# Kernel tuning notes

Hardware: AMD Instinct MI355X
Metric: run time of the kernel (lower is better)

The kernel has to match this reference:

```python
import jax, jax.numpy as jnp
import numpy as np

D_QK = 32  # out_channels // 8


def conv1x1(x, w, b):
    # x: [B,C,H,W], w: [O,C], b: [O] -> [B,O,H,W]
    return jnp.einsum('bchw,oc->bohw', x, w) + b[None, :, None, None]


def setup_inputs() -> dict:
    key = jax.random.key(0)
    ks = jax.random.split(key, 10)
    B, C, H, W = 4, 256, 64, 64
    in_ch, out_ch, attn_ch = 512, 256, 256
    s_in = 1.0 / np.sqrt(in_ch)
    s_at = 1.0 / np.sqrt(attn_ch)
    return {
        'ef': jax.random.normal(ks[0], (B, C, H, W), jnp.float32),
        'sf': jax.random.normal(ks[1], (B, C, H, W), jnp.float32),
        'Attn': jax.random.normal(ks[2], (B, attn_ch, H, W), jnp.float32),
        'Qw': jax.random.uniform(ks[3], (D_QK, in_ch), jnp.float32, -s_in, s_in),
        'Qb': jax.random.uniform(ks[4], (D_QK,), jnp.float32, -s_in, s_in),
        'Kw': jax.random.uniform(ks[5], (D_QK, attn_ch), jnp.float32, -s_at, s_at),
        'Kb': jax.random.uniform(ks[6], (D_QK,), jnp.float32, -s_at, s_at),
        'Vw': jax.random.uniform(ks[7], (out_ch, in_ch), jnp.float32, -s_in, s_in),
        'Vb': jax.random.uniform(ks[8], (out_ch,), jnp.float32, -s_in, s_in),
        'gamma': jnp.ones((1,), jnp.float32) * 0.25,
    }


def reference(ef, sf, Attn, Qw, Qb, Kw, Kb, Vw, Vb, gamma):
    B, C, H, W = ef.shape
    N = H * W
    x = jnp.concatenate((ef, sf), axis=1)  # [B, 2C, H, W]
    q = conv1x1(x, Qw, Qb).reshape(B, D_QK, N)         # [B, d, N]
    k = conv1x1(Attn, Kw, Kb).reshape(B, D_QK, N)      # [B, d, N]
    # scores[b, m, n] = sum_d q[b, d, m] * k[b, d, n]  (no 1/sqrt(d) scale)
    scores = jnp.einsum('bdm,bdn->bmn', q, k)
    attn = jax.nn.softmax(scores, axis=-1)             # [B, N, N]
    v = conv1x1(x, Vw, Vb).reshape(B, C, N)            # [B, C, N]
    # out[b, c, m] = sum_n v[b, c, n] * attn[b, m, n]
    out = jnp.einsum('bcn,bmn->bcm', v, attn).reshape(B, C, H, W)
    return gamma[0] * out + ef
```

## Files before the change

kernel.cpp:

```cpp
#include <hip/hip_runtime.h>
#include <hip/hip_bf16.h>

typedef short bf16x8 __attribute__((ext_vector_type(8)));
typedef float f32x4 __attribute__((ext_vector_type(4)));

#define MFMA16(a, b, c) __builtin_amdgcn_mfma_f32_16x16x32_bf16(a, b, c, 0, 0, 0)

#define NB 4
#define NC 256
#define NSP 4096
#define LOG2E 1.4426950408889634f

__device__ __forceinline__ unsigned short f2bf(float f) {
    return (unsigned short)((__float_as_uint(f) + 0x8000u) >> 16);
}
__device__ __forceinline__ unsigned pk2bf(float hi, float lo) {
    return __builtin_amdgcn_perm(__float_as_uint(hi) + 0x8000u,
                                 __float_as_uint(lo) + 0x8000u, 0x07060302u);
}

__global__ __launch_bounds__(256) void prep_w(
    const float* __restrict__ Qw, const float* __restrict__ Kw,
    const float* __restrict__ Vw,
    unsigned short* __restrict__ Qwbf, unsigned short* __restrict__ Kwbf,
    unsigned short* __restrict__ Vwbf)
{
    int i = blockIdx.x * 256 + threadIdx.x;
    {
        const float4* vs = (const float4*)(Vw + (size_t)i * 8);
        float4 a = vs[0], c = vs[1];
        int4 st;
        st.x = (int)pk2bf(a.y, a.x); st.y = (int)pk2bf(a.w, a.z);
        st.z = (int)pk2bf(c.y, c.x); st.w = (int)pk2bf(c.w, c.z);
        *(int4*)(Vwbf + (size_t)i * 8) = st;
    }
    if (i < 2048) {
        const float4* qs = (const float4*)(Qw + (size_t)i * 8);
        float4 a = qs[0], c = qs[1];
        int4 st;
        st.x = (int)pk2bf(a.y, a.x); st.y = (int)pk2bf(a.w, a.z);
        st.z = (int)pk2bf(c.y, c.x); st.w = (int)pk2bf(c.w, c.z);
        *(int4*)(Qwbf + (size_t)i * 8) = st;
    }
    if (i < 1024) {
        const float4* ks = (const float4*)(Kw + (size_t)i * 8);
        float4 a = ks[0], c = ks[1];
        int4 st;
        st.x = (int)pk2bf(a.y, a.x); st.y = (int)pk2bf(a.w, a.z);
        st.z = (int)pk2bf(c.y, c.x); st.w = (int)pk2bf(c.w, c.z);
        *(int4*)(Kwbf + (size_t)i * 8) = st;
    }
}

__global__ __launch_bounds__(256) void proj_fused(
    const float* __restrict__ ef, const float* __restrict__ sf,
    const float* __restrict__ attnp,
    const unsigned short* __restrict__ Qwbf, const float* __restrict__ Qb,
    const unsigned short* __restrict__ Kwbf, const float* __restrict__ Kb,
    const unsigned short* __restrict__ Vwbf, const float* __restrict__ Vb,
    unsigned short* __restrict__ qws, unsigned short* __restrict__ kws,
    unsigned short* __restrict__ vws)
{
    __shared__ __align__(16) unsigned short xt[32][72];

    int t = threadIdx.x;
    int w = t >> 6, lane = t & 63, quad = lane >> 4, l15 = lane & 15;
    int b = blockIdx.y;
    int ci = t & 63, sm = t >> 6;
    int mi = w >> 1, oh = w & 1;

    if (blockIdx.x < 128) {
        int mt = blockIdx.x, m0 = mt * 32;

        f32x4 zero = {0.f, 0.f, 0.f, 0.f};
        f32x4 acc[2][4];
#pragma unroll
        for (int m = 0; m < 2; ++m)
#pragma unroll
            for (int ot = 0; ot < 4; ++ot) acc[m][ot] = zero;
        f32x4 qacc = zero;

        const float* s0p = ef + ((size_t)(b * NC) + ci) * NSP + m0 + sm * 8;
        float4 x0 = *(const float4*)s0p;
        float4 x1 = *(const float4*)(s0p + 4);

        for (int c = 0; c < 8; ++c) {
            float4 n0 = x0, n1 = x1;
            if (c < 7) {
                int cn = c + 1;
                const float* sn = (cn < 4 ? ef : sf) +
                                  ((size_t)(b * NC) + (cn & 3) * 64 + ci) * NSP + m0 + sm * 8;
                n0 = *(const float4*)sn;
                n1 = *(const float4*)(sn + 4);
            }
            __syncthreads();
            unsigned short* xd = &xt[sm * 8][ci];
            xd[0]   = f2bf(x0.x); xd[72]  = f2bf(x0.y);
            xd[144] = f2bf(x0.z); xd[216] = f2bf(x0.w);
            xd[288] = f2bf(x1.x); xd[360] = f2bf(x1.y);
            xd[432] = f2bf(x1.z); xd[504] = f2bf(x1.w);
            __syncthreads();
            int ci0 = c * 64;
#pragma unroll
            for (int ks = 0; ks < 2; ++ks) {
                bf16x8 a0 = *(const bf16x8*)&xt[l15][ks * 32 + quad * 8];
                bf16x8 a1 = *(const bf16x8*)&xt[16 + l15][ks * 32 + quad * 8];
                bf16x8 bq = *(const bf16x8*)(Qwbf + (size_t)(oh * 16 + l15) * 512 + ci0 + ks * 32 + quad * 8);
                qacc = MFMA16(mi ? a1 : a0, bq, qacc);
#pragma unroll
                for (int ot = 0; ot < 4; ++ot) {
                    bf16x8 bv = *(const bf16x8*)(Vwbf + (size_t)(w * 64 + ot * 16 + l15) * 512 + ci0 + ks * 32 + quad * 8);
                    acc[0][ot] = MFMA16(a0, bv, acc[0][ot]);
                    acc[1][ot] = MFMA16(a1, bv, acc[1][ot]);
                }
            }
            x0 = n0; x1 = n1;
        }

#pragma unroll
        for (int ot = 0; ot < 4; ++ot) {
            int ch = w * 64 + ot * 16 + l15;
            float bias = Vb[ch];
            unsigned* vp = (unsigned*)(vws + ((size_t)((b * 128 + mt) * 256 + ch)) * 32);
#pragma unroll
            for (int r = 0; r < 4; ++r)
                vp[quad * 4 + r] = pk2bf(acc[1][ot][r] + bias, acc[0][ot][r] + bias);
        }

        int o = oh * 16 + l15;
        float bb = Qb[o];
#pragma unroll
        for (int r = 0; r < 4; ++r) {
            int m = m0 + mi * 16 + quad * 4 + r;
            qws[((size_t)(b * NSP) + m) * 32 + o] = f2bf((qacc[r] + bb) * LOG2E);
        }
    } else {
        int mt = blockIdx.x - 128, m0 = mt * 32;

        f32x4 acc = {0.f, 0.f, 0.f, 0.f};

        const float* s0p = attnp + ((size_t)(b * NC) + ci) * NSP + m0 + sm * 8;
        float4 x0 = *(const float4*)s0p;
        float4 x1 = *(const float4*)(s0p + 4);

        for (int c = 0; c < 4; ++c) {
            float4 n0 = x0, n1 = x1;
            if (c < 3) {
                const float* sn = attnp + ((size_t)(b * NC) + (c + 1) * 64 + ci) * NSP + m0 + sm * 8;
                n0 = *(const float4*)sn;
                n1 = *(const float4*)(sn + 4);
            }
            __syncthreads();
            unsigned short* xd = &xt[sm * 8][ci];
            xd[0]   = f2bf(x0.x); xd[72]  = f2bf(x0.y);
            xd[144] = f2bf(x0.z); xd[216] = f2bf(x0.w);
            xd[288] = f2bf(x1.x); xd[360] = f2bf(x1.y);
            xd[432] = f2bf(x1.z); xd[504] = f2bf(x1.w);
            __syncthreads();
            int ci0 = c * 64;
#pragma unroll
            for (int ks = 0; ks < 2; ++ks) {
                bf16x8 a  = *(const bf16x8*)&xt[mi * 16 + l15][ks * 32 + quad * 8];
                bf16x8 bk = *(const bf16x8*)(Kwbf + (size_t)(oh * 16 + l15) * 256 + ci0 + ks * 32 + quad * 8);
                acc = MFMA16(a, bk, acc);
            }
            x0 = n0; x1 = n1;
        }

        int o = oh * 16 + l15;
        float bb = Kb[o];
#pragma unroll
        for (int r = 0; r < 4; ++r) {
            int m = m0 + mi * 16 + quad * 4 + r;
            kws[((size_t)(b * NSP) + m) * 32 + o] = f2bf(acc[r] + bb);
        }
    }
}

__global__ __launch_bounds__(512, 2) void attention(
    const unsigned short* __restrict__ qws, const unsigned short* __restrict__ kws,
    const unsigned short* __restrict__ vws, const float* __restrict__ ef,
    const float* __restrict__ gamma, float* __restrict__ out)
{
    __shared__ __align__(16) unsigned short Plds[2][2][64 * 72];
    __shared__ float denl[2][64];

    int t = threadIdx.x;
    int g = t >> 8, tl = t & 255;
    int w = tl >> 6, lane = tl & 63, quad = lane >> 4, l15 = lane & 15;
    int b = blockIdx.x >> 6, m0 = (blockIdx.x & 63) << 6;

    const unsigned short* kbase = kws + (size_t)(b * NSP) * 32;
    const unsigned short* vbase = vws + (size_t)(b * 128) * 8192;

    bf16x8 qf = *(const bf16x8*)(qws + ((size_t)(b * NSP) + m0 + w * 16 + l15) * 32 + quad * 8);

    f32x4 zero = {0.f, 0.f, 0.f, 0.f};
    f32x4 acc[4][4];
#pragma unroll
    for (int i = 0; i < 4; ++i)
#pragma unroll
        for (int j = 0; j < 4; ++j) acc[i][j] = zero;
    float lp0 = 0.f, lp1 = 0.f, lp2 = 0.f, lp3 = 0.f;

    int tt0 = g * 64;
    bf16x8 kf[4];
#pragma unroll
    for (int j = 0; j < 4; ++j)
        kf[j] = *(const bf16x8*)(kbase + (size_t)((tt0 + (j >> 1)) * 32 + (j & 1) * 16 + l15) * 32 + quad * 8);
    bf16x8 vf[2][4];
#pragma unroll
    for (int h = 0; h < 2; ++h)
#pragma unroll
        for (int cc = 0; cc < 4; ++cc)
            vf[h][cc] = *(const bf16x8*)(vbase + (size_t)(tt0 + h) * 8192 + (w * 64 + cc * 16 + l15) * 32 + quad * 8);

    for (int it = 0; it < 32; ++it) {
        int buf = it & 1;
        f32x4 s0 = MFMA16(qf, kf[0], zero);
        f32x4 s1 = MFMA16(qf, kf[1], zero);
        f32x4 s2 = MFMA16(qf, kf[2], zero);
        f32x4 s3 = MFMA16(qf, kf[3], zero);

        float e0[4], e1[4], e2[4], e3[4];
#pragma unroll
        for (int r = 0; r < 4; ++r) {
            e0[r] = __builtin_amdgcn_exp2f(s0[r]);
            e1[r] = __builtin_amdgcn_exp2f(s1[r]);
            e2[r] = __builtin_amdgcn_exp2f(s2[r]);
            e3[r] = __builtin_amdgcn_exp2f(s3[r]);
        }
        lp0 += (e0[0] + e1[0]) + (e2[0] + e3[0]);
        lp1 += (e0[1] + e1[1]) + (e2[1] + e3[1]);
        lp2 += (e0[2] + e1[2]) + (e2[2] + e3[2]);
        lp3 += (e0[3] + e1[3]) + (e2[3] + e3[3]);

        unsigned short* pd = &Plds[g][buf][(w * 16 + quad * 4) * 72 + 2 * l15];
#pragma unroll
        for (int r = 0; r < 4; ++r) {
            *(unsigned*)(pd + r * 72)      = pk2bf(e1[r], e0[r]);
            *(unsigned*)(pd + r * 72 + 32) = pk2bf(e3[r], e2[r]);
        }

        int itn = it + 1 < 32 ? it + 1 : 31;
        int ttn = tt0 + 2 * itn;
#pragma unroll
        for (int j = 0; j < 4; ++j)
            kf[j] = *(const bf16x8*)(kbase + (size_t)((ttn + (j >> 1)) * 32 + (j & 1) * 16 + l15) * 32 + quad * 8);
        bf16x8 vfn[2][4];
#pragma unroll
        for (int h = 0; h < 2; ++h)
#pragma unroll
            for (int cc = 0; cc < 4; ++cc)
                vfn[h][cc] = *(const bf16x8*)(vbase + (size_t)(ttn + h) * 8192 + (w * 64 + cc * 16 + l15) * 32 + quad * 8);

        __syncthreads();

        __builtin_amdgcn_s_setprio(1);
#pragma unroll
        for (int h = 0; h < 2; ++h) {
            bf16x8 pa0 = *(const bf16x8*)&Plds[g][buf][(0  + l15) * 72 + h * 32 + quad * 8];
            bf16x8 pa1 = *(const bf16x8*)&Plds[g][buf][(16 + l15) * 72 + h * 32 + quad * 8];
            bf16x8 pa2 = *(const bf16x8*)&Plds[g][buf][(32 + l15) * 72 + h * 32 + quad * 8];
            bf16x8 pa3 = *(const bf16x8*)&Plds[g][buf][(48 + l15) * 72 + h * 32 + quad * 8];
#pragma unroll
            for (int cc = 0; cc < 4; ++cc) {
                acc[0][cc] = MFMA16(pa0, vf[h][cc], acc[0][cc]);
                acc[1][cc] = MFMA16(pa1, vf[h][cc], acc[1][cc]);
                acc[2][cc] = MFMA16(pa2, vf[h][cc], acc[2][cc]);
                acc[3][cc] = MFMA16(pa3, vf[h][cc], acc[3][cc]);
            }
        }
        __builtin_amdgcn_s_setprio(0);
#pragma unroll
        for (int h = 0; h < 2; ++h)
#pragma unroll
            for (int cc = 0; cc < 4; ++cc) vf[h][cc] = vfn[h][cc];
    }

    lp0 += __shfl_xor(lp0, 1); lp0 += __shfl_xor(lp0, 2); lp0 += __shfl_xor(lp0, 4); lp0 += __shfl_xor(lp0, 8);
    lp1 += __shfl_xor(lp1, 1); lp1 += __shfl_xor(lp1, 2); lp1 += __shfl_xor(lp1, 4); lp1 += __shfl_xor(lp1, 8);
    lp2 += __shfl_xor(lp2, 1); lp2 += __shfl_xor(lp2, 2); lp2 += __shfl_xor(lp2, 4); lp2 += __shfl_xor(lp2, 8);
    lp3 += __shfl_xor(lp3, 1); lp3 += __shfl_xor(lp3, 2); lp3 += __shfl_xor(lp3, 4); lp3 += __shfl_xor(lp3, 8);
    if (l15 == 0) {
        int base = w * 16 + quad * 4;
        denl[g][base + 0] = lp0; denl[g][base + 1] = lp1;
        denl[g][base + 2] = lp2; denl[g][base + 3] = lp3;
    }
    __syncthreads();

    float (*mrgO)[68] = (float (*)[68])&Plds[0][0][0];
    float gam = gamma[0];

#pragma unroll
    for (int half = 0; half < 2; ++half) {
        if (g == 1) {
#pragma unroll
            for (int qc = 0; qc < 4; ++qc)
#pragma unroll
                for (int c2 = 0; c2 < 2; ++c2)
                    *(f32x4*)&mrgO[w * 32 + c2 * 16 + l15][qc * 16 + quad * 4] = acc[qc][half * 2 + c2];
        }
        __syncthreads();
        if (g == 0) {
#pragma unroll
            for (int qc = 0; qc < 4; ++qc) {
                int qb = qc * 16 + quad * 4;
                float4 d0 = *(const float4*)&denl[0][qb];
                float4 d1 = *(const float4*)&denl[1][qb];
                float r0 = gam / (d0.x + d1.x), r1 = gam / (d0.y + d1.y);
                float r2 = gam / (d0.z + d1.z), r3 = gam / (d0.w + d1.w);
#pragma unroll
                for (int c2 = 0; c2 < 2; ++c2) {
                    int cc = half * 2 + c2;
                    int ch = w * 64 + cc * 16 + l15;
                    f32x4 part = *(const f32x4*)&mrgO[w * 32 + c2 * 16 + l15][qb];
                    size_t off = ((size_t)(b * NC + ch)) * NSP + m0 + qb;
                    float4 e = *(const float4*)(ef + off);
                    float4 o;
                    o.x = (acc[qc][cc][0] + part[0]) * r0 + e.x;
                    o.y = (acc[qc][cc][1] + part[1]) * r1 + e.y;
                    o.z = (acc[qc][cc][2] + part[2]) * r2 + e.z;
                    o.w = (acc[qc][cc][3] + part[3]) * r3 + e.w;
                    *(float4*)(out + off) = o;
                }
            }
        }
        __syncthreads();
    }
}

extern "C" void kernel_launch(void* const* d_in, const int* in_sizes, int n_in,
                              void* d_out, int out_size, void* d_ws, size_t ws_size,
                              hipStream_t stream) {
    const float* ef    = (const float*)d_in[0];
    const float* sf    = (const float*)d_in[1];
    const float* attn  = (const float*)d_in[2];
    const float* Qw    = (const float*)d_in[3];
    const float* Qb    = (const float*)d_in[4];
    const float* Kw    = (const float*)d_in[5];
    const float* Kb    = (const float*)d_in[6];
    const float* Vw    = (const float*)d_in[7];
    const float* Vb    = (const float*)d_in[8];
    const float* gamma = (const float*)d_in[9];
    float* out = (float*)d_out;

    unsigned short* qws  = (unsigned short*)d_ws;
    unsigned short* kws  = qws + (size_t)4 * 4096 * 32;
    unsigned short* vws  = kws + (size_t)4 * 4096 * 32;
    unsigned short* Qwbf = vws + (size_t)4 * 128 * 256 * 32;
    unsigned short* Kwbf = Qwbf + 32 * 512;
    unsigned short* Vwbf = Kwbf + 32 * 256;

    hipLaunchKernelGGL(prep_w, dim3(64), dim3(256), 0, stream,
                       Qw, Kw, Vw, Qwbf, Kwbf, Vwbf);
    hipLaunchKernelGGL(proj_fused, dim3(256, 4), dim3(256), 0, stream,
                       ef, sf, attn, Qwbf, Qb, Kwbf, Kb, Vwbf, Vb, qws, kws, vws);
    hipLaunchKernelGGL(attention, dim3(256), dim3(512), 0, stream,
                       qws, kws, vws, ef, gamma, out);
}
```

Before: 190.5 us.

## Split projection kernel, ping-pong V registers, and single-pass epilogue merge

Splits the fused Q/V/K projection into two separate kernels, so Q/V blocks and the lighter K blocks no longer share one grid. In the attention loop, a macro unrolled by two alternates between two V register buffers, which removes the per-iteration register copy; the s_setprio hints are dropped. The epilogue gets a dedicated full-size LDS merge buffer, so the two-half merge loop and its extra barriers become a single pass. This raises LDS use, which may cut occupancy below two blocks per CU, and adds one kernel launch.

```diff
diff --git a/kernel.cpp b/kernel.cpp
--- a/kernel.cpp
+++ b/kernel.cpp
@@ -52,81 +52,76 @@
     }
 }
 
-__global__ __launch_bounds__(256) void proj_fused(
+__global__ __launch_bounds__(256) void proj_qv(
     const float* __restrict__ ef, const float* __restrict__ sf,
-    const float* __restrict__ attnp,
     const unsigned short* __restrict__ Qwbf, const float* __restrict__ Qb,
-    const unsigned short* __restrict__ Kwbf, const float* __restrict__ Kb,
     const unsigned short* __restrict__ Vwbf, const float* __restrict__ Vb,
-    unsigned short* __restrict__ qws, unsigned short* __restrict__ kws,
-    unsigned short* __restrict__ vws)
+    unsigned short* __restrict__ qws, unsigned short* __restrict__ vws)
 {
     __shared__ __align__(16) unsigned short xt[32][72];
 
     int t = threadIdx.x;
     int w = t >> 6, lane = t & 63, quad = lane >> 4, l15 = lane & 15;
-    int b = blockIdx.y;
+    int mt = blockIdx.x, b = blockIdx.y, m0 = mt * 32;
     int ci = t & 63, sm = t >> 6;
     int mi = w >> 1, oh = w & 1;
 
-    if (blockIdx.x < 128) {
-        int mt = blockIdx.x, m0 = mt * 32;
-
-        f32x4 zero = {0.f, 0.f, 0.f, 0.f};
-        f32x4 acc[2][4];
-#pragma unroll
-        for (int m = 0; m < 2; ++m)
-#pragma unroll
-            for (int ot = 0; ot < 4; ++ot) acc[m][ot] = zero;
-        f32x4 qacc = zero;
-
-        const float* s0p = ef + ((size_t)(b * NC) + ci) * NSP + m0 + sm * 8;
-        float4 x0 = *(const float4*)s0p;
-        float4 x1 = *(const float4*)(s0p + 4);
-
-        for (int c = 0; c < 8; ++c) {
-            float4 n0 = x0, n1 = x1;
-            if (c < 7) {
-                int cn = c + 1;
-                const float* sn = (cn < 4 ? ef : sf) +
-                                  ((size_t)(b * NC) + (cn & 3) * 64 + ci) * NSP + m0 + sm * 8;
-                n0 = *(const float4*)sn;
-                n1 = *(const float4*)(sn + 4);
+    f32x4 zero = {0.f, 0.f, 0.f, 0.f};
+    f32x4 acc[2][4];
+#pragma unroll
+    for (int m = 0; m < 2; ++m)
+#pragma unroll
+        for (int ot = 0; ot < 4; ++ot) acc[m][ot] = zero;
+    f32x4 qacc = zero;
+
+    const float* s0p = ef + ((size_t)(b * NC) + ci) * NSP + m0 + sm * 8;
+    float4 x0 = *(const float4*)s0p;
+    float4 x1 = *(const float4*)(s0p + 4);
+
+    for (int c = 0; c < 8; ++c) {
+        float4 n0 = x0, n1 = x1;
+        if (c < 7) {
+            int cn = c + 1;
+            const float* sn = (cn < 4 ? ef : sf) +
+                              ((size_t)(b * NC) + (cn & 3) * 64 + ci) * NSP + m0 + sm * 8;
+            n0 = *(const float4*)sn;
+            n1 = *(const float4*)(sn + 4);
+        }
+        __syncthreads();
+        unsigned short* xd = &xt[sm * 8][ci];
+        xd[0]   = f2bf(x0.x); xd[72]  = f2bf(x0.y);
+        xd[144] = f2bf(x0.z); xd[216] = f2bf(x0.w);
+        xd[288] = f2bf(x1.x); xd[360] = f2bf(x1.y);
+        xd[432] = f2bf(x1.z); xd[504] = f2bf(x1.w);
+        __syncthreads();
+        int ci0 = c * 64;
+#pragma unroll
+        for (int ks = 0; ks < 2; ++ks) {
+            bf16x8 a0 = *(const bf16x8*)&xt[l15][ks * 32 + quad * 8];
+            bf16x8 a1 = *(const bf16x8*)&xt[16 + l15][ks * 32 + quad * 8];
+            bf16x8 bq = *(const bf16x8*)(Qwbf + (size_t)(oh * 16 + l15) * 512 + ci0 + ks * 32 + quad * 8);
+            qacc = MFMA16(mi ? a1 : a0, bq, qacc);
+#pragma unroll
+            for (int ot = 0; ot < 4; ++ot) {
+                bf16x8 bv = *(const bf16x8*)(Vwbf + (size_t)(w * 64 + ot * 16 + l15) * 512 + ci0 + ks * 32 + quad * 8);
+                acc[0][ot] = MFMA16(a0, bv, acc[0][ot]);
+                acc[1][ot] = MFMA16(a1, bv, acc[1][ot]);
             }
-            __syncthreads();
-            unsigned short* xd = &xt[sm * 8][ci];
-            xd[0]   = f2bf(x0.x); xd[72]  = f2bf(x0.y);
-            xd[144] = f2bf(x0.z); xd[216] = f2bf(x0.w);
-            xd[288] = f2bf(x1.x); xd[360] = f2bf(x1.y);
-            xd[432] = f2bf(x1.z); xd[504] = f2bf(x1.w);
-            __syncthreads();
-            int ci0 = c * 64;
-#pragma unroll
-            for (int ks = 0; ks < 2; ++ks) {
-                bf16x8 a0 = *(const bf16x8*)&xt[l15][ks * 32 + quad * 8];
-                bf16x8 a1 = *(const bf16x8*)&xt[16 + l15][ks * 32 + quad * 8];
-                bf16x8 bq = *(const bf16x8*)(Qwbf + (size_t)(oh * 16 + l15) * 512 + ci0 + ks * 32 + quad * 8);
-                qacc = MFMA16(mi ? a1 : a0, bq, qacc);
-#pragma unroll
-                for (int ot = 0; ot < 4; ++ot) {
-                    bf16x8 bv = *(const bf16x8*)(Vwbf + (size_t)(w * 64 + ot * 16 + l15) * 512 + ci0 + ks * 32 + quad * 8);
-                    acc[0][ot] = MFMA16(a0, bv, acc[0][ot]);
-                    acc[1][ot] = MFMA16(a1, bv, acc[1][ot]);
-                }
-            }
-            x0 = n0; x1 = n1;
-        }
-
-#pragma unroll
-        for (int ot = 0; ot < 4; ++ot) {
-            int ch = w * 64 + ot * 16 + l15;
-            float bias = Vb[ch];
-            unsigned* vp = (unsigned*)(vws + ((size_t)((b * 128 + mt) * 256 + ch)) * 32);
-#pragma unroll
-            for (int r = 0; r < 4; ++r)
-                vp[quad * 4 + r] = pk2bf(acc[1][ot][r] + bias, acc[0][ot][r] + bias);
-        }
-
+        }
+        x0 = n0; x1 = n1;
+    }
+
+#pragma unroll
+    for (int ot = 0; ot < 4; ++ot) {
+        int ch = w * 64 + ot * 16 + l15;
+        float bias = Vb[ch];
+        unsigned* vp = (unsigned*)(vws + ((size_t)((b * 128 + mt) * 256 + ch)) * 32);
+#pragma unroll
+        for (int r = 0; r < 4; ++r)
+            vp[quad * 4 + r] = pk2bf(acc[1][ot][r] + bias, acc[0][ot][r] + bias);
+    }
+
+    {
         int o = oh * 16 + l15;
         float bb = Qb[o];
 #pragma unroll
@@ -134,55 +129,121 @@
             int m = m0 + mi * 16 + quad * 4 + r;
             qws[((size_t)(b * NSP) + m) * 32 + o] = f2bf((qacc[r] + bb) * LOG2E);
         }
-    } else {
-        int mt = blockIdx.x - 128, m0 = mt * 32;
-
-        f32x4 acc = {0.f, 0.f, 0.f, 0.f};
-
-        const float* s0p = attnp + ((size_t)(b * NC) + ci) * NSP + m0 + sm * 8;
-        float4 x0 = *(const float4*)s0p;
-        float4 x1 = *(const float4*)(s0p + 4);
-
-        for (int c = 0; c < 4; ++c) {
-            float4 n0 = x0, n1 = x1;
-            if (c < 3) {
-                const float* sn = attnp + ((size_t)(b * NC) + (c + 1) * 64 + ci) * NSP + m0 + sm * 8;
-                n0 = *(const float4*)sn;
-                n1 = *(const float4*)(sn + 4);
-            }
-            __syncthreads();
-            unsigned short* xd = &xt[sm * 8][ci];
-            xd[0]   = f2bf(x0.x); xd[72]  = f2bf(x0.y);
-            xd[144] = f2bf(x0.z); xd[216] = f2bf(x0.w);
-            xd[288] = f2bf(x1.x); xd[360] = f2bf(x1.y);
-            xd[432] = f2bf(x1.z); xd[504] = f2bf(x1.w);
-            __syncthreads();
-            int ci0 = c * 64;
-#pragma unroll
-            for (int ks = 0; ks < 2; ++ks) {
-                bf16x8 a  = *(const bf16x8*)&xt[mi * 16 + l15][ks * 32 + quad * 8];
-                bf16x8 bk = *(const bf16x8*)(Kwbf + (size_t)(oh * 16 + l15) * 256 + ci0 + ks * 32 + quad * 8);
-                acc = MFMA16(a, bk, acc);
-            }
-            x0 = n0; x1 = n1;
-        }
-
-        int o = oh * 16 + l15;
-        float bb = Kb[o];
-#pragma unroll
-        for (int r = 0; r < 4; ++r) {
-            int m = m0 + mi * 16 + quad * 4 + r;
-            kws[((size_t)(b * NSP) + m) * 32 + o] = f2bf(acc[r] + bb);
-        }
-    }
-}
+    }
+}
+
+__global__ __launch_bounds__(256) void proj_k(
+    const float* __restrict__ attn,
+    const unsigned short* __restrict__ Kwbf, const float* __restrict__ Kb,
+    unsigned short* __restrict__ kws)
+{
+    __shared__ __align__(16) unsigned short xt[32][72];
+
+    int t = threadIdx.x;
+    int w = t >> 6, lane = t & 63, quad = lane >> 4, l15 = lane & 15;
+    int mt = blockIdx.x, b = blockIdx.y, m0 = mt * 32;
+    int ci = t & 63, sm = t >> 6;
+    int mi = w >> 1, oh = w & 1;
+
+    f32x4 acc = {0.f, 0.f, 0.f, 0.f};
+
+    const float* s0p = attn + ((size_t)(b * NC) + ci) * NSP + m0 + sm * 8;
+    float4 x0 = *(const float4*)s0p;
+    float4 x1 = *(const float4*)(s0p + 4);
+
+    for (int c = 0; c < 4; ++c) {
+        float4 n0 = x0, n1 = x1;
+        if (c < 3) {
+            const float* sn = attn + ((size_t)(b * NC) + (c + 1) * 64 + ci) * NSP + m0 + sm * 8;
+            n0 = *(const float4*)sn;
+            n1 = *(const float4*)(sn + 4);
+        }
+        __syncthreads();
+        unsigned short* xd = &xt[sm * 8][ci];
+        xd[0]   = f2bf(x0.x); xd[72]  = f2bf(x0.y);
+        xd[144] = f2bf(x0.z); xd[216] = f2bf(x0.w);
+        xd[288] = f2bf(x1.x); xd[360] = f2bf(x1.y);
+        xd[432] = f2bf(x1.z); xd[504] = f2bf(x1.w);
+        __syncthreads();
+        int ci0 = c * 64;
+#pragma unroll
+        for (int ks = 0; ks < 2; ++ks) {
+            bf16x8 a  = *(const bf16x8*)&xt[mi * 16 + l15][ks * 32 + quad * 8];
+            bf16x8 bk = *(const bf16x8*)(Kwbf + (size_t)(oh * 16 + l15) * 256 + ci0 + ks * 32 + quad * 8);
+            acc = MFMA16(a, bk, acc);
+        }
+        x0 = n0; x1 = n1;
+    }
+
+    int o = oh * 16 + l15;
+    float bb = Kb[o];
+#pragma unroll
+    for (int r = 0; r < 4; ++r) {
+        int m = m0 + mi * 16 + quad * 4 + r;
+        kws[((size_t)(b * NSP) + m) * 32 + o] = f2bf(acc[r] + bb);
+    }
+}
+
+
+#define ATT_ITER(IT, VCUR, VNXT)                                              \
+    {                                                                         \
+        int buf = (IT) & 1;                                                   \
+        f32x4 s0 = MFMA16(qf, kf[0], zero);                                   \
+        f32x4 s1 = MFMA16(qf, kf[1], zero);                                   \
+        f32x4 s2 = MFMA16(qf, kf[2], zero);                                   \
+        f32x4 s3 = MFMA16(qf, kf[3], zero);                                   \
+        float e0[4], e1[4], e2[4], e3[4];                                     \
+        _Pragma("unroll")                                                     \
+        for (int r = 0; r < 4; ++r) {                                         \
+            e0[r] = __builtin_amdgcn_exp2f(s0[r]);                            \
+            e1[r] = __builtin_amdgcn_exp2f(s1[r]);                            \
+            e2[r] = __builtin_amdgcn_exp2f(s2[r]);                            \
+            e3[r] = __builtin_amdgcn_exp2f(s3[r]);                            \
+        }                                                                     \
+        lp0 += (e0[0] + e1[0]) + (e2[0] + e3[0]);                             \
+        lp1 += (e0[1] + e1[1]) + (e2[1] + e3[1]);                             \
+        lp2 += (e0[2] + e1[2]) + (e2[2] + e3[2]);                             \
+        lp3 += (e0[3] + e1[3]) + (e2[3] + e3[3]);                             \
+        unsigned short* pd = &Plds[g][buf][(w * 16 + quad * 4) * 72 + 2 * l15]; \
+        _Pragma("unroll")                                                     \
+        for (int r = 0; r < 4; ++r) {                                         \
+            *(unsigned*)(pd + r * 72)      = pk2bf(e1[r], e0[r]);             \
+            *(unsigned*)(pd + r * 72 + 32) = pk2bf(e3[r], e2[r]);             \
+        }                                                                     \
+        int itn = (IT) + 1 < 32 ? (IT) + 1 : 31;                              \
+        int ttn = tt0 + 2 * itn;                                              \
+        _Pragma("unroll")                                                     \
+        for (int j = 0; j < 4; ++j)                                           \
+            kf[j] = *(const bf16x8*)(kbase + (size_t)((ttn + (j >> 1)) * 32 + (j & 1) * 16 + l15) * 32 + quad * 8); \
+        _Pragma("unroll")                                                     \
+        for (int h = 0; h < 2; ++h)                                           \
+            _Pragma("unroll")                                                 \
+            for (int cc = 0; cc < 4; ++cc)                                    \
+                VNXT[h][cc] = *(const bf16x8*)(vbase + (size_t)(ttn + h) * 8192 + (w * 64 + cc * 16 + l15) * 32 + quad * 8); \
+        __syncthreads();                                                      \
+        _Pragma("unroll")                                                     \
+        for (int h = 0; h < 2; ++h) {                                         \
+            bf16x8 pa0 = *(const bf16x8*)&Plds[g][buf][(0  + l15) * 72 + h * 32 + quad * 8]; \
+            bf16x8 pa1 = *(const bf16x8*)&Plds[g][buf][(16 + l15) * 72 + h * 32 + quad * 8]; \
+            bf16x8 pa2 = *(const bf16x8*)&Plds[g][buf][(32 + l15) * 72 + h * 32 + quad * 8]; \
+            bf16x8 pa3 = *(const bf16x8*)&Plds[g][buf][(48 + l15) * 72 + h * 32 + quad * 8]; \
+            _Pragma("unroll")                                                 \
+            for (int cc = 0; cc < 4; ++cc) {                                  \
+                acc[0][cc] = MFMA16(pa0, VCUR[h][cc], acc[0][cc]);            \
+                acc[1][cc] = MFMA16(pa1, VCUR[h][cc], acc[1][cc]);            \
+                acc[2][cc] = MFMA16(pa2, VCUR[h][cc], acc[2][cc]);            \
+                acc[3][cc] = MFMA16(pa3, VCUR[h][cc], acc[3][cc]);            \
+            }                                                                 \
+        }                                                                     \
+    }
 
 __global__ __launch_bounds__(512, 2) void attention(
     const unsigned short* __restrict__ qws, const unsigned short* __restrict__ kws,
     const unsigned short* __restrict__ vws, const float* __restrict__ ef,
     const float* __restrict__ gamma, float* __restrict__ out)
 {
-    __shared__ __align__(16) unsigned short Plds[2][2][64 * 72];
+    __shared__ unsigned short Plds[2][2][64 * 72];
+    __shared__ float mrg[256][68];
     __shared__ float denl[2][64];
 
     int t = threadIdx.x;
@@ -208,74 +269,16 @@
 #pragma unroll
     for (int j = 0; j < 4; ++j)
         kf[j] = *(const bf16x8*)(kbase + (size_t)((tt0 + (j >> 1)) * 32 + (j & 1) * 16 + l15) * 32 + quad * 8);
-    bf16x8 vf[2][4];
+    bf16x8 vfA[2][4], vfB[2][4];
 #pragma unroll
     for (int h = 0; h < 2; ++h)
 #pragma unroll
         for (int cc = 0; cc < 4; ++cc)
-            vf[h][cc] = *(const bf16x8*)(vbase + (size_t)(tt0 + h) * 8192 + (w * 64 + cc * 16 + l15) * 32 + quad * 8);
-
-    for (int it = 0; it < 32; ++it) {
-        int buf = it & 1;
-        f32x4 s0 = MFMA16(qf, kf[0], zero);
-        f32x4 s1 = MFMA16(qf, kf[1], zero);
-        f32x4 s2 = MFMA16(qf, kf[2], zero);
-        f32x4 s3 = MFMA16(qf, kf[3], zero);
-
-        float e0[4], e1[4], e2[4], e3[4];
-#pragma unroll
-        for (int r = 0; r < 4; ++r) {
-            e0[r] = __builtin_amdgcn_exp2f(s0[r]);
-            e1[r] = __builtin_amdgcn_exp2f(s1[r]);
-            e2[r] = __builtin_amdgcn_exp2f(s2[r]);
-            e3[r] = __builtin_amdgcn_exp2f(s3[r]);
-        }
-        lp0 += (e0[0] + e1[0]) + (e2[0] + e3[0]);
-        lp1 += (e0[1] + e1[1]) + (e2[1] + e3[1]);
-        lp2 += (e0[2] + e1[2]) + (e2[2] + e3[2]);
-        lp3 += (e0[3] + e1[3]) + (e2[3] + e3[3]);
-
-        unsigned short* pd = &Plds[g][buf][(w * 16 + quad * 4) * 72 + 2 * l15];
-#pragma unroll
-        for (int r = 0; r < 4; ++r) {
-            *(unsigned*)(pd + r * 72)      = pk2bf(e1[r], e0[r]);
-            *(unsigned*)(pd + r * 72 + 32) = pk2bf(e3[r], e2[r]);
-        }
-
-        int itn = it + 1 < 32 ? it + 1 : 31;
-        int ttn = tt0 + 2 * itn;
-#pragma unroll
-        for (int j = 0; j < 4; ++j)
-            kf[j] = *(const bf16x8*)(kbase + (size_t)((ttn + (j >> 1)) * 32 + (j & 1) * 16 + l15) * 32 + quad * 8);
-        bf16x8 vfn[2][4];
-#pragma unroll
-        for (int h = 0; h < 2; ++h)
-#pragma unroll
-            for (int cc = 0; cc < 4; ++cc)
-                vfn[h][cc] = *(const bf16x8*)(vbase + (size_t)(ttn + h) * 8192 + (w * 64 + cc * 16 + l15) * 32 + quad * 8);
-
-        __syncthreads();
-
-        __builtin_amdgcn_s_setprio(1);
-#pragma unroll
-        for (int h = 0; h < 2; ++h) {
-            bf16x8 pa0 = *(const bf16x8*)&Plds[g][buf][(0  + l15) * 72 + h * 32 + quad * 8];
-            bf16x8 pa1 = *(const bf16x8*)&Plds[g][buf][(16 + l15) * 72 + h * 32 + quad * 8];
-            bf16x8 pa2 = *(const bf16x8*)&Plds[g][buf][(32 + l15) * 72 + h * 32 + quad * 8];
-            bf16x8 pa3 = *(const bf16x8*)&Plds[g][buf][(48 + l15) * 72 + h * 32 + quad * 8];
-#pragma unroll
-            for (int cc = 0; cc < 4; ++cc) {
-                acc[0][cc] = MFMA16(pa0, vf[h][cc], acc[0][cc]);
-                acc[1][cc] = MFMA16(pa1, vf[h][cc], acc[1][cc]);
-                acc[2][cc] = MFMA16(pa2, vf[h][cc], acc[2][cc]);
-                acc[3][cc] = MFMA16(pa3, vf[h][cc], acc[3][cc]);
-            }
-        }
-        __builtin_amdgcn_s_setprio(0);
-#pragma unroll
-        for (int h = 0; h < 2; ++h)
-#pragma unroll
-            for (int cc = 0; cc < 4; ++cc) vf[h][cc] = vfn[h][cc];
+            vfA[h][cc] = *(const bf16x8*)(vbase + (size_t)(tt0 + h) * 8192 + (w * 64 + cc * 16 + l15) * 32 + quad * 8);
+
+    for (int it2 = 0; it2 < 16; ++it2) {
+        ATT_ITER(2 * it2,     vfA, vfB);
+        ATT_ITER(2 * it2 + 1, vfB, vfA);
     }
 
     lp0 += __shfl_xor(lp0, 1); lp0 += __shfl_xor(lp0, 2); lp0 += __shfl_xor(lp0, 4); lp0 += __shfl_xor(lp0, 8);
@@ -287,46 +290,38 @@
         denl[g][base + 0] = lp0; denl[g][base + 1] = lp1;
         denl[g][base + 2] = lp2; denl[g][base + 3] = lp3;
     }
+    if (g == 1) {
+#pragma unroll
+        for (int qc = 0; qc < 4; ++qc)
+#pragma unroll
+            for (int cc = 0; cc < 4; ++cc)
+                *(f32x4*)&mrg[w * 64 + cc * 16 + l15][qc * 16 + quad * 4] = acc[qc][cc];
+    }
     __syncthreads();
 
-    float (*mrgO)[68] = (float (*)[68])&Plds[0][0][0];
-    float gam = gamma[0];
-
-#pragma unroll
-    for (int half = 0; half < 2; ++half) {
-        if (g == 1) {
-#pragma unroll
-            for (int qc = 0; qc < 4; ++qc)
-#pragma unroll
-                for (int c2 = 0; c2 < 2; ++c2)
-                    *(f32x4*)&mrgO[w * 32 + c2 * 16 + l15][qc * 16 + quad * 4] = acc[qc][half * 2 + c2];
-        }
-        __syncthreads();
-        if (g == 0) {
-#pragma unroll
-            for (int qc = 0; qc < 4; ++qc) {
-                int qb = qc * 16 + quad * 4;
-                float4 d0 = *(const float4*)&denl[0][qb];
-                float4 d1 = *(const float4*)&denl[1][qb];
-                float r0 = gam / (d0.x + d1.x), r1 = gam / (d0.y + d1.y);
-                float r2 = gam / (d0.z + d1.z), r3 = gam / (d0.w + d1.w);
-#pragma unroll
-                for (int c2 = 0; c2 < 2; ++c2) {
-                    int cc = half * 2 + c2;
-                    int ch = w * 64 + cc * 16 + l15;
-                    f32x4 part = *(const f32x4*)&mrgO[w * 32 + c2 * 16 + l15][qb];
-                    size_t off = ((size_t)(b * NC + ch)) * NSP + m0 + qb;
-                    float4 e = *(const float4*)(ef + off);
-                    float4 o;
-                    o.x = (acc[qc][cc][0] + part[0]) * r0 + e.x;
-                    o.y = (acc[qc][cc][1] + part[1]) * r1 + e.y;
-                    o.z = (acc[qc][cc][2] + part[2]) * r2 + e.z;
-                    o.w = (acc[qc][cc][3] + part[3]) * r3 + e.w;
-                    *(float4*)(out + off) = o;
-                }
+    if (g == 0) {
+        float gam = gamma[0];
+#pragma unroll
+        for (int qc = 0; qc < 4; ++qc) {
+            int qb = qc * 16 + quad * 4;
+            float4 d0 = *(const float4*)&denl[0][qb];
+            float4 d1 = *(const float4*)&denl[1][qb];
+            float r0 = gam / (d0.x + d1.x), r1 = gam / (d0.y + d1.y);
+            float r2 = gam / (d0.z + d1.z), r3 = gam / (d0.w + d1.w);
+#pragma unroll
+            for (int cc = 0; cc < 4; ++cc) {
+                int ch = w * 64 + cc * 16 + l15;
+                f32x4 part = *(const f32x4*)&mrg[ch][qb];
+                size_t off = ((size_t)(b * NC + ch)) * NSP + m0 + qb;
+                float4 e = *(const float4*)(ef + off);
+                float4 o;
+                o.x = (acc[qc][cc][0] + part[0]) * r0 + e.x;
+                o.y = (acc[qc][cc][1] + part[1]) * r1 + e.y;
+                o.z = (acc[qc][cc][2] + part[2]) * r2 + e.z;
+                o.w = (acc[qc][cc][3] + part[3]) * r3 + e.w;
+                *(float4*)(out + off) = o;
             }
         }
-        __syncthreads();
     }
 }
 
@@ -354,8 +349,10 @@
 
     hipLaunchKernelGGL(prep_w, dim3(64), dim3(256), 0, stream,
                        Qw, Kw, Vw, Qwbf, Kwbf, Vwbf);
-    hipLaunchKernelGGL(proj_fused, dim3(256, 4), dim3(256), 0, stream,
-                       ef, sf, attn, Qwbf, Qb, Kwbf, Kb, Vwbf, Vb, qws, kws, vws);
+    hipLaunchKernelGGL(proj_qv, dim3(128, 4), dim3(256), 0, stream,
+                       ef, sf, Qwbf, Qb, Vwbf, Vb, qws, vws);
+    hipLaunchKernelGGL(proj_k, dim3(128, 4), dim3(256), 0, stream,
+                       attn, Kwbf, Kb, kws);
     hipLaunchKernelGGL(attention, dim3(256), dim3(512), 0, stream,
                        qws, kws, vws, ef, gamma, out);
 }
```

Result: faster. 178.6 us (-6.2%).
